# Kernel tuning notes

Hardware: AMD Instinct MI355X
Metric: run time of the kernel (lower is better)

The kernel has to match this reference:

```python
import jax, jax.numpy as jnp
import numpy as np

N, D, NUM_CLASSES = 8192, 64, 16
EPS = 1e-7


def setup_inputs() -> dict:
    key = jax.random.key(0)
    k1, k2 = jax.random.split(key)
    raw = jax.random.normal(k1, (N, D), dtype=jnp.float32)
    # project into the open Poincare ball: norm < 0.9
    nrm = jnp.linalg.norm(raw, axis=-1, keepdims=True)
    points = raw * (0.9 / (1.0 + nrm))
    labels = jax.random.randint(k2, (N,), 0, NUM_CLASSES, dtype=jnp.int64)
    return {"points": points, "labels": labels}


def _poincare_dist_matrix(x):
    # d(x,y) = arccosh(1 + 2||x-y||^2 / ((1-||x||^2)(1-||y||^2)))
    sq = jnp.sum(x * x, axis=-1)                      # [N]
    sqdist = jnp.maximum(sq[:, None] + sq[None, :] - 2.0 * (x @ x.T), 0.0)  # [N,N]
    denom = jnp.maximum((1.0 - sq)[:, None] * (1.0 - sq)[None, :], EPS)
    arg = jnp.maximum(1.0 + 2.0 * sqdist / denom, 1.0 + EPS)
    return jnp.arccosh(arg)


def reference(points, labels):
    d = _poincare_dist_matrix(points)                 # [N,N]
    logits = -d
    n = logits.shape[0]
    diag = jnp.eye(n, dtype=bool)
    neg_inf = jnp.finfo(logits.dtype).min
    # log A_i = logsumexp_{a != i} (-d_ia)
    logA = jax.nn.logsumexp(jnp.where(diag, neg_inf, logits), axis=1)  # [N]
    pos = (labels[:, None] == labels[None, :]) & (~diag)               # [N,N]
    P = jnp.sum(pos, axis=1).astype(logits.dtype)                      # [N]
    p_sum = jnp.sum(jnp.where(pos, logits - logA[:, None], 0.0), axis=1)
    return jnp.sum(-p_sum / P)
```

## Files before the change

### kernel.cpp

```cpp
#include <hip/hip_runtime.h>

#define NPTS 8192
#define DIM 64
#define EPSF 1e-7f
#define LN2F 0.69314718055994531f
#define NBLK 1056

typedef unsigned short u16;
typedef __attribute__((ext_vector_type(8))) short bf16x8;
typedef __attribute__((ext_vector_type(8))) unsigned short u16x8;
typedef __attribute__((ext_vector_type(4))) float f32x4;
typedef __attribute__((ext_vector_type(2))) float f32x2;

__global__ void prep_kernel(const float* __restrict__ x, const int* __restrict__ labels,
                            u16* __restrict__ hi,
                            float4* __restrict__ meta,
                            float* __restrict__ out) {
    int g = blockIdx.x * blockDim.x + threadIdx.x;
    int row = g >> 3, sub = g & 7;
    const float* xp = x + row * DIM + sub * 8;
    float v[8];
    float s = 0.f;
#pragma unroll
    for (int k = 0; k < 8; k++) { v[k] = xp[k]; s = fmaf(v[k], v[k], s); }
    s += __shfl_xor(s, 1);
    s += __shfl_xor(s, 2);
    s += __shfl_xor(s, 4);
    u16x8 h;
#pragma unroll
    for (int k = 0; k < 8; k++) {
        unsigned int bits = __float_as_uint(v[k]);
        unsigned int r = bits + 0x7FFFu + ((bits >> 16) & 1u);
        h[k] = (u16)(r >> 16);
    }
    *(u16x8*)(hi + row * DIM + sub * 8) = h;
    if (sub == 0) {
        float r = 1.0f / (1.0f - s);
        meta[row] = make_float4(-0.5f * s, r, -4.0f * r, (float)labels[row]);
    }
    if (g == 3) out[0] = 0.f;
}

__device__ __forceinline__ int cumtiles(int b) { return 65 * b - b * b; }

__global__ void __launch_bounds__(256, 4) pair_mfma(
        const u16* __restrict__ hi,
        const float4* __restrict__ meta,
        float* __restrict__ Pi, float* __restrict__ Pj) {
    __shared__ float slabS[4][128], slabT[4][128];

    int tid = threadIdx.x;
    int wave = tid >> 6, lane = tid & 63;
    int quad = lane >> 4, l15 = lane & 15;

    int bid2 = blockIdx.x;
    int bid = bid2 >> 1;
    int half = bid2 & 1;
    int by = (int)((65.0f - __builtin_amdgcn_sqrtf(4225.0f - 4.0f * (float)bid)) * 0.5f);
    while (cumtiles(by + 1) <= bid) by++;
    while (cumtiles(by) > bid) by--;
    int off = bid - cumtiles(by);
    int bx = 2 * by + off;
    bool full = (off >= 2);

    int i0 = bx * 128 + wave * 32;
    int j0 = by * 256;
    int jbase = j0 + half * 128;

    bf16x8 a_hi[2][2];
#pragma unroll
    for (int it = 0; it < 2; it++)
#pragma unroll
        for (int ks = 0; ks < 2; ks++) {
            int aoff = (i0 + it * 16 + l15) * DIM + ks * 32 + quad * 8;
            a_hi[it][ks] = *(const bf16x8*)(hi + aoff);
        }

    f32x4 hsqi4[2];
    f32x2 rcp2[4];
    float labi[8];
#pragma unroll
    for (int it = 0; it < 2; it++)
#pragma unroll
        for (int r = 0; r < 4; r++) {
            float4 m = meta[i0 + it * 16 + quad * 4 + r];
            hsqi4[it][r] = m.x;
            rcp2[it * 2 + (r >> 1)][r & 1] = m.y;
            labi[it * 4 + r] = m.w;
        }

    if (full) {
        slabS[wave][lane] = 0.f;       slabT[wave][lane] = 0.f;
        slabS[wave][lane + 64] = 0.f;  slabT[wave][lane + 64] = 0.f;
    }

    f32x2 Sx2[4], Tx2[4];
#pragma unroll
    for (int k = 0; k < 4; k++) { Sx2[k] = (f32x2){0.f, 0.f}; Tx2[k] = (f32x2){0.f, 0.f}; }

    bf16x8 bh[2][2];
    float4 mjb[2];
    {
        int boff = (jbase + l15) * DIM + quad * 8;
        bh[0][0] = *(const bf16x8*)(hi + boff);
        bh[0][1] = *(const bf16x8*)(hi + boff + 32);
        mjb[0] = meta[jbase + l15];
    }

#pragma unroll 2
    for (int t = 0; t < 8; t++) {
        int cur = t & 1, nxt = cur ^ 1;
        if (t < 7) {
            int jgn = jbase + (t + 1) * 16 + l15;
            int boff = jgn * DIM + quad * 8;
            bh[nxt][0] = *(const bf16x8*)(hi + boff);
            bh[nxt][1] = *(const bf16x8*)(hi + boff + 32);
            mjb[nxt] = meta[jgn];
        }
        float4 mj = mjb[cur];

        f32x2 sSum = (f32x2){0.f, 0.f}, tSum = (f32x2){0.f, 0.f};
#pragma unroll
        for (int it = 0; it < 2; it++) {
            f32x4 acc = hsqi4[it] + mj.x;
            acc = __builtin_amdgcn_mfma_f32_16x16x32_bf16(a_hi[it][0], bh[cur][0], acc, 0, 0, 0);
            acc = __builtin_amdgcn_mfma_f32_16x16x32_bf16(a_hi[it][1], bh[cur][1], acc, 0, 0, 0);

#pragma unroll
            for (int g = 0; g < 2; g++) {
                f32x2 D = (f32x2){acc[2 * g], acc[2 * g + 1]};
                f32x2 u = (D * rcp2[it * 2 + g]) * mj.z;
                u = __builtin_elementwise_max(u, (f32x2){EPSF, EPSF});
                f32x2 arg = u * u + (u + u);
                f32x2 srt = (f32x2){__builtin_amdgcn_sqrtf(arg.x), __builtin_amdgcn_sqrtf(arg.y)};
                f32x2 opu = u + 1.0f;
                f32x2 st = opu - srt;
                f32x2 w1 = opu + srt;
                f32x2 l2;
                l2.x = __builtin_amdgcn_logf(w1.x);
                l2.y = __builtin_amdgcn_logf(w1.y);
                f32x2 tv;
                tv.x = (mj.w == labi[it * 4 + 2 * g]) ? l2.x : 0.0f;
                tv.y = (mj.w == labi[it * 4 + 2 * g + 1]) ? l2.y : 0.0f;
                Sx2[it * 2 + g] += st;
                Tx2[it * 2 + g] += tv;
                sSum += st;
                tSum += tv;
            }
        }

        if (full) {
            float pS = sSum.x + sSum.y, pT = tSum.x + tSum.y;
            pS += __shfl_xor(pS, 16); pS += __shfl_xor(pS, 32);
            pT += __shfl_xor(pT, 16); pT += __shfl_xor(pT, 32);
            if (quad == 0) {
                int c = t * 16 + l15;
                slabS[wave][c] += pS;
                slabT[wave][c] += pT;
            }
        }
    }

    float Sx[8], Tx[8];
#pragma unroll
    for (int k = 0; k < 4; k++) {
        Sx[2 * k] = Sx2[k].x; Sx[2 * k + 1] = Sx2[k].y;
        Tx[2 * k] = Tx2[k].x; Tx[2 * k + 1] = Tx2[k].y;
    }
#pragma unroll
    for (int r = 0; r < 8; r++) {
#pragma unroll
        for (int m = 1; m < 16; m <<= 1) {
            Sx[r] += __shfl_xor(Sx[r], m);
            Tx[r] += __shfl_xor(Tx[r], m);
        }
    }
    float* PiB = Pi + (size_t)bid2 * 256;
    if (l15 == 0) {
#pragma unroll
        for (int it = 0; it < 2; it++)
#pragma unroll
            for (int r = 0; r < 4; r++) {
                int rowb = wave * 32 + it * 16 + quad * 4 + r;
                PiB[rowb] = Sx[it * 4 + r];
                PiB[128 + rowb] = Tx[it * 4 + r];
            }
    }

    if (full) {
        __syncthreads();
        float* PjB = Pj + (size_t)bid2 * 256;
        if (tid < 128) {
            PjB[tid] = slabS[0][tid] + slabS[1][tid] + slabS[2][tid] + slabS[3][tid];
        } else {
            int c = tid - 128;
            PjB[tid] = slabT[0][c] + slabT[1][c] + slabT[2][c] + slabT[3][c];
        }
    }
}

__global__ void __launch_bounds__(256) finalize_kernel(
        const float* __restrict__ Pi, const float* __restrict__ Pj,
        const int* __restrict__ labels, float* __restrict__ out) {
    __shared__ int hist[16][16];
    __shared__ float cntf[16];
    __shared__ float redS[4][64], redT[4][64];
    int tid = threadIdx.x;
    hist[tid >> 4][tid & 15] = 0;
    __syncthreads();
    int rep = tid & 15;
    for (int i = tid; i < NPTS; i += 256)
        atomicAdd(&hist[rep][labels[i]], 1);
    __syncthreads();
    if (tid < 16) {
        int s = 0;
#pragma unroll
        for (int k = 0; k < 16; k++) s += hist[k][tid];
        cntf[tid] = (float)(s - 1);
    }

    int slice = tid >> 6, pl = tid & 63;
    int i = blockIdx.x * 64 + pl;
    int bx = i >> 7, r = i & 127;
    float s = 0.f, t = 0.f;
    for (int by = slice; by <= (bx >> 1); by += 4) {
        int c2 = (cumtiles(by) + (bx - 2 * by)) * 512;
        s += Pi[c2 + r] + Pi[c2 + 256 + r];
        t += Pi[c2 + 128 + r] + Pi[c2 + 384 + r];
    }
    int byj = bx >> 1, half = bx & 1;
    int jmax = 64 - 2 * byj;
    int cbase = cumtiles(byj);
    for (int off = 2 + slice; off < jmax; off += 4) {
        int c2 = ((cbase + off) * 2 + half) * 256;
        s += Pj[c2 + r];
        t += Pj[c2 + 128 + r];
    }
    redS[slice][pl] = s;
    redT[slice][pl] = t;
    __syncthreads();
    if (tid < 64) {
        float S = redS[0][tid] + redS[1][tid] + redS[2][tid] + redS[3][tid];
        float T = redT[0][tid] + redT[1][tid] + redT[2][tid] + redT[3][tid];
        float s0 = __builtin_amdgcn_sqrtf(EPSF * (2.0f + EPSF));
        float st0 = 1.0f + EPSF - s0;
        float l20 = __builtin_amdgcn_logf(1.0f + EPSF + s0);
        int ii = blockIdx.x * 64 + tid;
        float loss = __logf(S - st0) + (T - l20) * LN2F / cntf[labels[ii]];
#pragma unroll
        for (int m = 1; m < 64; m <<= 1) loss += __shfl_xor(loss, m);
        if (tid == 0) atomicAdd(out, loss);
    }
}

extern "C" void kernel_launch(void* const* d_in, const int* in_sizes, int n_in,
                              void* d_out, int out_size, void* d_ws, size_t ws_size,
                              hipStream_t stream) {
    const float* x = (const float*)d_in[0];
    const int* labels = (const int*)d_in[1];

    u16* hi = (u16*)d_ws;
    float4* meta = (float4*)(hi + NPTS * DIM);
    float* Pi = (float*)(meta + NPTS);
    float* Pj = Pi + 2 * NBLK * 256;

    prep_kernel<<<(NPTS * 8) / 256, 256, 0, stream>>>(x, labels, hi, meta, (float*)d_out);

    pair_mfma<<<2 * NBLK, 256, 0, stream>>>(hi, meta, Pi, Pj);

    finalize_kernel<<<NPTS / 64, 256, 0, stream>>>(Pi, Pj, labels, (float*)d_out);
}
```

Baseline: 104.6 us.

## Split pair blocks into single-wave blocks and replace per-pair logs with products

Each 4-wave block becomes four independent 64-thread blocks, which removes the shared-memory cross-wave reduction and the __syncthreads. Each wave starts its column loop at a staggered offset so concurrent waves read different rows. The per-pair log of the positive terms is replaced by a running product with a single log per row or column, which cuts transcendental work. In exchange the partial buffers grow, finalize reads four times as many column partials, and the product of up to dozens of values can overflow or lose precision.

```diff
diff --git a/kernel.cpp b/kernel.cpp
--- a/kernel.cpp
+++ b/kernel.cpp
@@ -43,19 +43,20 @@
 
 __device__ __forceinline__ int cumtiles(int b) { return 65 * b - b * b; }
 
-__global__ void __launch_bounds__(256, 4) pair_mfma(
+__global__ void __launch_bounds__(64, 4) pair_mfma(
         const u16* __restrict__ hi,
         const float4* __restrict__ meta,
         float* __restrict__ Pi, float* __restrict__ Pj) {
-    __shared__ float slabS[4][128], slabT[4][128];
-
-    int tid = threadIdx.x;
-    int wave = tid >> 6, lane = tid & 63;
+    __shared__ float slabS[128], slabT[128];
+
+    int lane = threadIdx.x;
     int quad = lane >> 4, l15 = lane & 15;
 
-    int bid2 = blockIdx.x;
+    int b = blockIdx.x;
+    int w = b & 3;
+    int bid2 = b >> 2;
+    int half = bid2 & 1;
     int bid = bid2 >> 1;
-    int half = bid2 & 1;
     int by = (int)((65.0f - __builtin_amdgcn_sqrtf(4225.0f - 4.0f * (float)bid)) * 0.5f);
     while (cumtiles(by + 1) <= bid) by++;
     while (cumtiles(by) > bid) by--;
@@ -63,9 +64,9 @@
     int bx = 2 * by + off;
     bool full = (off >= 2);
 
-    int i0 = bx * 128 + wave * 32;
-    int j0 = by * 256;
-    int jbase = j0 + half * 128;
+    int i0 = bx * 128 + w * 32;
+    int jbase = by * 256 + half * 128;
+    int offs = b & 7;
 
     bf16x8 a_hi[2][2];
 #pragma unroll
@@ -89,29 +90,26 @@
             labi[it * 4 + r] = m.w;
         }
 
-    if (full) {
-        slabS[wave][lane] = 0.f;       slabT[wave][lane] = 0.f;
-        slabS[wave][lane + 64] = 0.f;  slabT[wave][lane + 64] = 0.f;
-    }
-
-    f32x2 Sx2[4], Tx2[4];
-#pragma unroll
-    for (int k = 0; k < 4; k++) { Sx2[k] = (f32x2){0.f, 0.f}; Tx2[k] = (f32x2){0.f, 0.f}; }
+    f32x2 Sx2[4], Tp2[4];
+#pragma unroll
+    for (int k = 0; k < 4; k++) { Sx2[k] = (f32x2){0.f, 0.f}; Tp2[k] = (f32x2){1.f, 1.f}; }
 
     bf16x8 bh[2][2];
     float4 mjb[2];
     {
-        int boff = (jbase + l15) * DIM + quad * 8;
+        int jg0 = jbase + offs * 16 + l15;
+        int boff = jg0 * DIM + quad * 8;
         bh[0][0] = *(const bf16x8*)(hi + boff);
         bh[0][1] = *(const bf16x8*)(hi + boff + 32);
-        mjb[0] = meta[jbase + l15];
+        mjb[0] = meta[jg0];
     }
 
 #pragma unroll 2
     for (int t = 0; t < 8; t++) {
         int cur = t & 1, nxt = cur ^ 1;
+        int t2 = (t + offs) & 7;
         if (t < 7) {
-            int jgn = jbase + (t + 1) * 16 + l15;
+            int jgn = jbase + (((t + 1 + offs) & 7) * 16) + l15;
             int boff = jgn * DIM + quad * 8;
             bh[nxt][0] = *(const bf16x8*)(hi + boff);
             bh[nxt][1] = *(const bf16x8*)(hi + boff + 32);
@@ -119,7 +117,8 @@
         }
         float4 mj = mjb[cur];
 
-        f32x2 sSum = (f32x2){0.f, 0.f}, tSum = (f32x2){0.f, 0.f};
+        f32x2 sSum = (f32x2){0.f, 0.f};
+        f32x2 tProd = (f32x2){1.f, 1.f};
 #pragma unroll
         for (int it = 0; it < 2; it++) {
             f32x4 acc = hsqi4[it] + mj.x;
@@ -136,28 +135,24 @@
                 f32x2 opu = u + 1.0f;
                 f32x2 st = opu - srt;
                 f32x2 w1 = opu + srt;
-                f32x2 l2;
-                l2.x = __builtin_amdgcn_logf(w1.x);
-                l2.y = __builtin_amdgcn_logf(w1.y);
-                f32x2 tv;
-                tv.x = (mj.w == labi[it * 4 + 2 * g]) ? l2.x : 0.0f;
-                tv.y = (mj.w == labi[it * 4 + 2 * g + 1]) ? l2.y : 0.0f;
+                f32x2 sel;
+                sel.x = (mj.w == labi[it * 4 + 2 * g]) ? w1.x : 1.0f;
+                sel.y = (mj.w == labi[it * 4 + 2 * g + 1]) ? w1.y : 1.0f;
                 Sx2[it * 2 + g] += st;
-                Tx2[it * 2 + g] += tv;
+                Tp2[it * 2 + g] *= sel;
                 sSum += st;
-                tSum += tv;
+                tProd *= sel;
             }
         }
 
-        if (full) {
-            float pS = sSum.x + sSum.y, pT = tSum.x + tSum.y;
-            pS += __shfl_xor(pS, 16); pS += __shfl_xor(pS, 32);
-            pT += __shfl_xor(pT, 16); pT += __shfl_xor(pT, 32);
-            if (quad == 0) {
-                int c = t * 16 + l15;
-                slabS[wave][c] += pS;
-                slabT[wave][c] += pT;
-            }
+        float pS = sSum.x + sSum.y;
+        float pT = __builtin_amdgcn_logf(tProd.x * tProd.y);
+        pS += __shfl_xor(pS, 16); pS += __shfl_xor(pS, 32);
+        pT += __shfl_xor(pT, 16); pT += __shfl_xor(pT, 32);
+        if (quad == 0) {
+            int c = t2 * 16 + l15;
+            slabS[c] = pS;
+            slabT[c] = pT;
         }
     }
 
@@ -165,7 +160,8 @@
 #pragma unroll
     for (int k = 0; k < 4; k++) {
         Sx[2 * k] = Sx2[k].x; Sx[2 * k + 1] = Sx2[k].y;
-        Tx[2 * k] = Tx2[k].x; Tx[2 * k + 1] = Tx2[k].y;
+        Tx[2 * k] = __builtin_amdgcn_logf(Tp2[k].x);
+        Tx[2 * k + 1] = __builtin_amdgcn_logf(Tp2[k].y);
     }
 #pragma unroll
     for (int r = 0; r < 8; r++) {
@@ -175,27 +171,24 @@
             Tx[r] += __shfl_xor(Tx[r], m);
         }
     }
-    float* PiB = Pi + (size_t)bid2 * 256;
+    float* PiB = Pi + (size_t)b * 64;
     if (l15 == 0) {
 #pragma unroll
         for (int it = 0; it < 2; it++)
 #pragma unroll
             for (int r = 0; r < 4; r++) {
-                int rowb = wave * 32 + it * 16 + quad * 4 + r;
+                int rowb = it * 16 + quad * 4 + r;
                 PiB[rowb] = Sx[it * 4 + r];
-                PiB[128 + rowb] = Tx[it * 4 + r];
+                PiB[32 + rowb] = Tx[it * 4 + r];
             }
     }
 
     if (full) {
-        __syncthreads();
-        float* PjB = Pj + (size_t)bid2 * 256;
-        if (tid < 128) {
-            PjB[tid] = slabS[0][tid] + slabS[1][tid] + slabS[2][tid] + slabS[3][tid];
-        } else {
-            int c = tid - 128;
-            PjB[tid] = slabT[0][c] + slabT[1][c] + slabT[2][c] + slabT[3][c];
-        }
+        float* PjB = Pj + (size_t)b * 256;
+        PjB[lane]       = slabS[lane];
+        PjB[lane + 64]  = slabS[lane + 64];
+        PjB[lane + 128] = slabT[lane];
+        PjB[lane + 192] = slabT[lane + 64];
     }
 }
 
@@ -221,20 +214,28 @@
 
     int slice = tid >> 6, pl = tid & 63;
     int i = blockIdx.x * 64 + pl;
-    int bx = i >> 7, r = i & 127;
+    int bx = i >> 7;
+    int r128 = i & 127;
+    int wq = r128 >> 5;
+    int r32 = i & 31;
     float s = 0.f, t = 0.f;
     for (int by = slice; by <= (bx >> 1); by += 4) {
-        int c2 = (cumtiles(by) + (bx - 2 * by)) * 512;
-        s += Pi[c2 + r] + Pi[c2 + 256 + r];
-        t += Pi[c2 + 128 + r] + Pi[c2 + 384 + r];
-    }
-    int byj = bx >> 1, half = bx & 1;
+        int bidb = cumtiles(by) + (bx - 2 * by);
+        int b0 = (bidb * 2) * 4 + wq;
+        int b1 = (bidb * 2 + 1) * 4 + wq;
+        s += Pi[(size_t)b0 * 64 + r32] + Pi[(size_t)b1 * 64 + r32];
+        t += Pi[(size_t)b0 * 64 + 32 + r32] + Pi[(size_t)b1 * 64 + 32 + r32];
+    }
+    int byj = bx >> 1, halfj = bx & 1;
     int jmax = 64 - 2 * byj;
     int cbase = cumtiles(byj);
     for (int off = 2 + slice; off < jmax; off += 4) {
-        int c2 = ((cbase + off) * 2 + half) * 256;
-        s += Pj[c2 + r];
-        t += Pj[c2 + 128 + r];
+        int bb = ((cbase + off) * 2 + halfj) * 4;
+#pragma unroll
+        for (int w2 = 0; w2 < 4; w2++) {
+            s += Pj[(size_t)(bb + w2) * 256 + r128];
+            t += Pj[(size_t)(bb + w2) * 256 + 128 + r128];
+        }
     }
     redS[slice][pl] = s;
     redT[slice][pl] = t;
@@ -262,11 +263,11 @@
     u16* hi = (u16*)d_ws;
     float4* meta = (float4*)(hi + NPTS * DIM);
     float* Pi = (float*)(meta + NPTS);
-    float* Pj = Pi + 2 * NBLK * 256;
+    float* Pj = Pi + (size_t)8 * NBLK * 64;
 
     prep_kernel<<<(NPTS * 8) / 256, 256, 0, stream>>>(x, labels, hi, meta, (float*)d_out);
 
-    pair_mfma<<<2 * NBLK, 256, 0, stream>>>(hi, meta, Pi, Pj);
+    pair_mfma<<<8 * NBLK, 64, 0, stream>>>(hi, meta, Pi, Pj);
 
     finalize_kernel<<<NPTS / 64, 256, 0, stream>>>(Pi, Pj, labels, (float*)d_out);
 }
```

Measured after the change: 107.5 us. 2.7% more time.
